# Optimization experiments

Hardware: AMD Instinct MI355X
Metric: run time of the kernel (lower is better)

The kernel has to match this reference:

```python
import jax, jax.numpy as jnp
import numpy as np

B, T, D, H = 256, 256, 384, 64  # batch, seq (BLOCK_SIZE), D_MODEL, HEAD_SIZE


def setup_inputs() -> dict:
    key = jax.random.key(0)
    k1, k2, k3, k4 = jax.random.split(key, 4)
    x = jax.random.normal(k1, (B, T, D), dtype=jnp.float32)
    # nn.Linear(D, H, bias=False): weight [H, D]; we store transposed [D, H] for x @ W
    Wq = jax.random.normal(k2, (D, H), dtype=jnp.float32) * (1.0 / np.sqrt(D))
    Wk = jax.random.normal(k3, (D, H), dtype=jnp.float32) * (1.0 / np.sqrt(D))
    Wv = jax.random.normal(k4, (D, H), dtype=jnp.float32) * (1.0 / np.sqrt(D))
    return {"x": x, "Wq": Wq, "Wk": Wk, "Wv": Wv}


def reference(x, Wq, Wk, Wv):
    # x: [B, T, D]
    q = x @ Wq  # [B, T, H]
    k = x @ Wk  # [B, T, H]
    v = x @ Wv  # [B, T, H]
    scale = 1.0 / jnp.sqrt(jnp.asarray(k.shape[-1], dtype=x.dtype))
    wei = jnp.einsum('bth,bsh->bts', q, k) * scale  # [B, T, T]
    causal = jnp.tril(jnp.ones((x.shape[1], x.shape[1]), dtype=bool))
    wei = jnp.where(causal, wei, -jnp.inf)
    wei = jax.nn.softmax(wei, axis=-1)
    # dropout is identity in eval mode (deterministic reference)
    out = jnp.einsum('bts,bsh->bth', wei, v)  # [B, T, H]
    return out
```

## Files before the change

### kernel.cpp

```cpp
#include <hip/hip_runtime.h>

#define BATCH 256
#define TT 256
#define DD 384
#define HH 64
#define SCALE 0.125f
#define SHIFT 14.0f

typedef __attribute__((ext_vector_type(8))) short short8;
typedef __attribute__((ext_vector_type(4))) float floatx4;

#define KS_STRIDE 72
#define QS_STRIDE 72
#define VT_STRIDE 264
#define PS_STRIDE 40
#define WELEMS (3 * DD * HH)

__device__ __forceinline__ unsigned short f2bf(float f) {
    unsigned int u = __float_as_uint(f);
    u += 0x7fffu + ((u >> 16) & 1u);
    return (unsigned short)(u >> 16);
}
__device__ __forceinline__ float bf2f(unsigned short u) {
    return __uint_as_float(((unsigned int)u) << 16);
}

__device__ __forceinline__ void gld_lds16(const void* g, void* ldst) {
    __builtin_amdgcn_global_load_lds(
        (__attribute__((address_space(1))) void*)(unsigned long long)g,
        (__attribute__((address_space(3))) void*)(unsigned int)(unsigned long long)ldst,
        16, 0, 0);
}

__device__ __forceinline__ short8 cvt8(float4 f0, float4 f1) {
    short8 a;
    a[0] = (short)f2bf(f0.x); a[1] = (short)f2bf(f0.y);
    a[2] = (short)f2bf(f0.z); a[3] = (short)f2bf(f0.w);
    a[4] = (short)f2bf(f1.x); a[5] = (short)f2bf(f1.y);
    a[6] = (short)f2bf(f1.z); a[7] = (short)f2bf(f1.w);
    return a;
}

__global__ void pack_w_kernel(const float* __restrict__ wq,
                              const float* __restrict__ wk,
                              const float* __restrict__ wv,
                              unsigned short* __restrict__ wf) {
    int idx = blockIdx.x * 256 + threadIdx.x;
    if (idx >= WELEMS) return;
    int j = idx & 7;
    int lane = (idx >> 3) & 63;
    int nt = (idx >> 9) & 3;
    int rem = idx >> 11;
    int mat = rem % 3;
    int ch = rem / 3;
    int l16 = lane & 15, q = lane >> 4;
    int h = 16 * nt + l16;
    int d = 32 * ch + 8 * q + j;
    const float* w = (mat == 0) ? wq : (mat == 1) ? wk : wv;
    wf[idx] = f2bf(w[d * HH + h]);
}

__global__ __launch_bounds__(512, 2)
void fused_kernel(const float* __restrict__ x, const unsigned short* __restrict__ wfrag,
                  float* __restrict__ out) {
    __shared__ __align__(16) union LdsU {
        unsigned short w[WELEMS];
        struct {
            unsigned short ks[TT * KS_STRIDE];
            unsigned short vt[HH * VT_STRIDE];
            unsigned short q[TT * QS_STRIDE];
            unsigned short p[8][16 * PS_STRIDE];
        } s;
    } U;

    const int b = blockIdx.x;
    const int tid = threadIdx.x;
    const int wave = tid >> 6;
    const int lane = tid & 63;
    const int quad = lane >> 4;
    const int l16 = lane & 15;

    const float* xb = x + (size_t)b * TT * DD;

    const float* xr0 = xb + (size_t)(32 * wave + l16) * DD + 8 * quad;
    const float* xr1 = xr0 + (size_t)16 * DD;

    floatx4 cq[2][4] = {};
    floatx4 ck[2][4] = {};
    floatx4 cv[2][4] = {};

    float4 xfA[4], xfB[4];

    xfA[0] = *(const float4*)(xr0);
    xfA[1] = *(const float4*)(xr0 + 4);
    xfA[2] = *(const float4*)(xr1);
    xfA[3] = *(const float4*)(xr1 + 4);

    #pragma unroll
    for (int t = 0; t < 18; ++t) {
        int grp = wave * 18 + t;
        gld_lds16(wfrag + (size_t)grp * 512 + lane * 8, U.w + grp * 512);
    }

    __syncthreads();

    #define GEMM_BODY(CUR, NXT, CH, PREF)                                          \
        {                                                                          \
            if (PREF) {                                                            \
                const float* p0_ = xr0 + ((CH) + 1) * 32;                          \
                const float* p1_ = xr1 + ((CH) + 1) * 32;                          \
                NXT[0] = *(const float4*)(p0_);                                    \
                NXT[1] = *(const float4*)(p0_ + 4);                                \
                NXT[2] = *(const float4*)(p1_);                                    \
                NXT[3] = *(const float4*)(p1_ + 4);                                \
            }                                                                      \
            short8 wf_[12];                                                        \
            _Pragma("unroll")                                                      \
            for (int i = 0; i < 12; ++i)                                           \
                wf_[i] = *(const short8*)(U.w + (size_t)((CH) * 12 + i) * 512 + lane * 8); \
            short8 a0 = cvt8(CUR[0], CUR[1]);                                      \
            short8 a1 = cvt8(CUR[2], CUR[3]);                                      \
            _Pragma("unroll")                                                      \
            for (int nt = 0; nt < 4; ++nt) {                                       \
                cq[0][nt] = __builtin_amdgcn_mfma_f32_16x16x32_bf16(a0, wf_[nt], cq[0][nt], 0, 0, 0);      \
                cq[1][nt] = __builtin_amdgcn_mfma_f32_16x16x32_bf16(a1, wf_[nt], cq[1][nt], 0, 0, 0);      \
                ck[0][nt] = __builtin_amdgcn_mfma_f32_16x16x32_bf16(a0, wf_[4 + nt], ck[0][nt], 0, 0, 0);  \
                ck[1][nt] = __builtin_amdgcn_mfma_f32_16x16x32_bf16(a1, wf_[4 + nt], ck[1][nt], 0, 0, 0);  \
                cv[0][nt] = __builtin_amdgcn_mfma_f32_16x16x32_bf16(a0, wf_[8 + nt], cv[0][nt], 0, 0, 0);  \
                cv[1][nt] = __builtin_amdgcn_mfma_f32_16x16x32_bf16(a1, wf_[8 + nt], cv[1][nt], 0, 0, 0);  \
            }                                                                      \
        }

    #pragma unroll 1
    for (int t = 0; t < 6; ++t) {
        GEMM_BODY(xfA, xfB, 2 * t, 1);
        GEMM_BODY(xfB, xfA, 2 * t + 1, (t < 5));
    }
    #undef GEMM_BODY

    __syncthreads();

    #pragma unroll
    for (int mi = 0; mi < 2; ++mi)
      #pragma unroll
      for (int nt = 0; nt < 4; ++nt)
        #pragma unroll
        for (int r = 0; r < 4; ++r) {
            int row = 32 * wave + 16 * mi + 4 * quad + r;
            int col = 16 * nt + l16;
            U.s.q[row * QS_STRIDE + col] = f2bf(cq[mi][nt][r]);
            U.s.ks[row * KS_STRIDE + col] = f2bf(ck[mi][nt][r]);
            U.s.vt[col * VT_STRIDE + row] = f2bf(cv[mi][nt][r]);
        }

    __syncthreads();

    floatx4 o[2][4] = {};
    float l_run[2][4] = {{0.f, 0.f, 0.f, 0.f}, {0.f, 0.f, 0.f, 0.f}};
    unsigned short* psw = U.s.p[wave];

    #pragma unroll
    for (int gi = 0; gi < 2; ++gi) {
        int g = gi ? (15 - wave) : wave;
        int gr0 = 16 * g;
        short8 aq0 = *(const short8*)(U.s.q + (size_t)(gr0 + l16) * QS_STRIDE + quad * 8);
        short8 aq1 = *(const short8*)(U.s.q + (size_t)(gr0 + l16) * QS_STRIDE + 32 + quad * 8);
        int clast = g >> 1;
        for (int c = 0; c <= clast; ++c) {
            floatx4 s[2] = {};
            #pragma unroll
            for (int ni = 0; ni < 2; ++ni) {
                const unsigned short* kbase =
                    U.s.ks + (size_t)(32 * c + 16 * ni + l16) * KS_STRIDE + quad * 8;
                s[ni] = __builtin_amdgcn_mfma_f32_16x16x32_bf16(aq0, *(const short8*)(kbase), s[ni], 0, 0, 0);
                s[ni] = __builtin_amdgcn_mfma_f32_16x16x32_bf16(aq1, *(const short8*)(kbase + 32), s[ni], 0, 0, 0);
            }
            bool partial = (c == clast);
            #pragma unroll
            for (int r = 0; r < 4; ++r) {
                int row = gr0 + 4 * quad + r;
                float p0 = __expf(s[0][r] * SCALE - SHIFT);
                float p1 = __expf(s[1][r] * SCALE - SHIFT);
                if (partial) {
                    if (32 * c + l16 > row) p0 = 0.f;
                    if (32 * c + 16 + l16 > row) p1 = 0.f;
                }
                unsigned short b0 = f2bf(p0), b1 = f2bf(p1);
                l_run[gi][r] += bf2f(b0) + bf2f(b1);
                psw[(4 * quad + r) * PS_STRIDE + l16] = b0;
                psw[(4 * quad + r) * PS_STRIDE + 16 + l16] = b1;
            }
            short8 ap = *(const short8*)(psw + l16 * PS_STRIDE + quad * 8);
            #pragma unroll
            for (int nt = 0; nt < 4; ++nt) {
                short8 bv = *(const short8*)(U.s.vt + (size_t)(16 * nt + l16) * VT_STRIDE + 32 * c + quad * 8);
                o[gi][nt] = __builtin_amdgcn_mfma_f32_16x16x32_bf16(ap, bv, o[gi][nt], 0, 0, 0);
            }
        }
    }

    float* outb = out + (size_t)b * TT * HH;
    #pragma unroll
    for (int gi = 0; gi < 2; ++gi) {
        int g = gi ? (15 - wave) : wave;
        #pragma unroll
        for (int r = 0; r < 4; ++r) {
            float l = l_run[gi][r];
            l += __shfl_xor(l, 1);
            l += __shfl_xor(l, 2);
            l += __shfl_xor(l, 4);
            l += __shfl_xor(l, 8);
            l_run[gi][r] = l;
        }
        #pragma unroll
        for (int nt = 0; nt < 4; ++nt)
          #pragma unroll
          for (int r = 0; r < 4; ++r) {
            int row = 16 * g + 4 * quad + r;
            outb[(size_t)row * HH + 16 * nt + l16] = o[gi][nt][r] / l_run[gi][r];
          }
    }
}

extern "C" void kernel_launch(void* const* d_in, const int* in_sizes, int n_in,
                              void* d_out, int out_size, void* d_ws, size_t ws_size,
                              hipStream_t stream) {
    const float* x  = (const float*)d_in[0];
    const float* wq = (const float*)d_in[1];
    const float* wk = (const float*)d_in[2];
    const float* wv = (const float*)d_in[3];
    unsigned short* wf = (unsigned short*)d_ws;
    float* o = (float*)d_out;

    pack_w_kernel<<<(WELEMS + 255) / 256, 256, 0, stream>>>(wq, wk, wv, wf);
    fused_kernel<<<BATCH, 512, 0, stream>>>(x, wf, o);
}
```

Baseline: 169.1 us.

## Fuse weight packing into main kernel and deepen x prefetch

Removes the separate weight-packing kernel launch. Each block now reads fp32 Wq/Wk/Wv straight from global memory, converts them to bf16 and writes them into the MFMA fragment layout in LDS. The x prefetch is reworked to keep two chunks in flight. The final normalization uses a reciprocal multiply instead of a divide. The cost is that all 256 blocks redo the weight conversion with strided scalar global loads, where before they did a single async global-to-LDS copy of pre-packed data.

```diff
diff --git a/kernel.cpp b/kernel.cpp
--- a/kernel.cpp
+++ b/kernel.cpp
@@ -23,13 +23,6 @@
 }
 __device__ __forceinline__ float bf2f(unsigned short u) {
     return __uint_as_float(((unsigned int)u) << 16);
-}
-
-__device__ __forceinline__ void gld_lds16(const void* g, void* ldst) {
-    __builtin_amdgcn_global_load_lds(
-        (__attribute__((address_space(1))) void*)(unsigned long long)g,
-        (__attribute__((address_space(3))) void*)(unsigned int)(unsigned long long)ldst,
-        16, 0, 0);
 }
 
 __device__ __forceinline__ short8 cvt8(float4 f0, float4 f1) {
@@ -41,27 +34,11 @@
     return a;
 }
 
-__global__ void pack_w_kernel(const float* __restrict__ wq,
-                              const float* __restrict__ wk,
-                              const float* __restrict__ wv,
-                              unsigned short* __restrict__ wf) {
-    int idx = blockIdx.x * 256 + threadIdx.x;
-    if (idx >= WELEMS) return;
-    int j = idx & 7;
-    int lane = (idx >> 3) & 63;
-    int nt = (idx >> 9) & 3;
-    int rem = idx >> 11;
-    int mat = rem % 3;
-    int ch = rem / 3;
-    int l16 = lane & 15, q = lane >> 4;
-    int h = 16 * nt + l16;
-    int d = 32 * ch + 8 * q + j;
-    const float* w = (mat == 0) ? wq : (mat == 1) ? wk : wv;
-    wf[idx] = f2bf(w[d * HH + h]);
-}
-
 __global__ __launch_bounds__(512, 2)
-void fused_kernel(const float* __restrict__ x, const unsigned short* __restrict__ wfrag,
+void fused_kernel(const float* __restrict__ x,
+                  const float* __restrict__ wq,
+                  const float* __restrict__ wk,
+                  const float* __restrict__ wv,
                   float* __restrict__ out) {
     __shared__ __align__(16) union LdsU {
         unsigned short w[WELEMS];
@@ -95,31 +72,46 @@
     xfA[1] = *(const float4*)(xr0 + 4);
     xfA[2] = *(const float4*)(xr1);
     xfA[3] = *(const float4*)(xr1 + 4);
-
-    #pragma unroll
-    for (int t = 0; t < 18; ++t) {
-        int grp = wave * 18 + t;
-        gld_lds16(wfrag + (size_t)grp * 512 + lane * 8, U.w + grp * 512);
+    xfB[0] = *(const float4*)(xr0 + 32);
+    xfB[1] = *(const float4*)(xr0 + 36);
+    xfB[2] = *(const float4*)(xr1 + 32);
+    xfB[3] = *(const float4*)(xr1 + 36);
+
+    for (int g = 0; g < 18; ++g) {
+        int gidx = g * 512 + tid;
+        int laneg = gidx & 63;
+        int nt = (gidx >> 6) & 3;
+        int rem = gidx >> 8;
+        int mat = rem % 3;
+        int ch = rem / 3;
+        int l16g = laneg & 15, qg = laneg >> 4;
+        const float* w = (mat == 0) ? wq : (mat == 1) ? wk : wv;
+        const float* src = w + (size_t)(32 * ch + 8 * qg) * HH + 16 * nt + l16g;
+        short8 pk;
+        #pragma unroll
+        for (int j = 0; j < 8; ++j)
+            pk[j] = (short)f2bf(src[(size_t)j * HH]);
+        *(short8*)(U.w + (size_t)gidx * 8) = pk;
     }
 
     __syncthreads();
 
-    #define GEMM_BODY(CUR, NXT, CH, PREF)                                          \
+    #define GEMM_BODY(BUF, CH)                                                     \
         {                                                                          \
-            if (PREF) {                                                            \
-                const float* p0_ = xr0 + ((CH) + 1) * 32;                          \
-                const float* p1_ = xr1 + ((CH) + 1) * 32;                          \
-                NXT[0] = *(const float4*)(p0_);                                    \
-                NXT[1] = *(const float4*)(p0_ + 4);                                \
-                NXT[2] = *(const float4*)(p1_);                                    \
-                NXT[3] = *(const float4*)(p1_ + 4);                                \
+            short8 a0 = cvt8(BUF[0], BUF[1]);                                      \
+            short8 a1 = cvt8(BUF[2], BUF[3]);                                      \
+            if ((CH) + 2 < 12) {                                                   \
+                const float* p0_ = xr0 + ((CH) + 2) * 32;                          \
+                const float* p1_ = xr1 + ((CH) + 2) * 32;                          \
+                BUF[0] = *(const float4*)(p0_);                                    \
+                BUF[1] = *(const float4*)(p0_ + 4);                                \
+                BUF[2] = *(const float4*)(p1_);                                    \
+                BUF[3] = *(const float4*)(p1_ + 4);                                \
             }                                                                      \
             short8 wf_[12];                                                        \
             _Pragma("unroll")                                                      \
             for (int i = 0; i < 12; ++i)                                           \
                 wf_[i] = *(const short8*)(U.w + (size_t)((CH) * 12 + i) * 512 + lane * 8); \
-            short8 a0 = cvt8(CUR[0], CUR[1]);                                      \
-            short8 a1 = cvt8(CUR[2], CUR[3]);                                      \
             _Pragma("unroll")                                                      \
             for (int nt = 0; nt < 4; ++nt) {                                       \
                 cq[0][nt] = __builtin_amdgcn_mfma_f32_16x16x32_bf16(a0, wf_[nt], cq[0][nt], 0, 0, 0);      \
@@ -133,8 +125,8 @@
 
     #pragma unroll 1
     for (int t = 0; t < 6; ++t) {
-        GEMM_BODY(xfA, xfB, 2 * t, 1);
-        GEMM_BODY(xfB, xfA, 2 * t + 1, (t < 5));
+        GEMM_BODY(xfA, 2 * t);
+        GEMM_BODY(xfB, 2 * t + 1);
     }
     #undef GEMM_BODY
 
@@ -203,6 +195,7 @@
     #pragma unroll
     for (int gi = 0; gi < 2; ++gi) {
         int g = gi ? (15 - wave) : wave;
+        float linv[4];
         #pragma unroll
         for (int r = 0; r < 4; ++r) {
             float l = l_run[gi][r];
@@ -210,14 +203,14 @@
             l += __shfl_xor(l, 2);
             l += __shfl_xor(l, 4);
             l += __shfl_xor(l, 8);
-            l_run[gi][r] = l;
+            linv[r] = 1.0f / l;
         }
         #pragma unroll
         for (int nt = 0; nt < 4; ++nt)
           #pragma unroll
           for (int r = 0; r < 4; ++r) {
             int row = 16 * g + 4 * quad + r;
-            outb[(size_t)row * HH + 16 * nt + l16] = o[gi][nt][r] / l_run[gi][r];
+            outb[(size_t)row * HH + 16 * nt + l16] = o[gi][nt][r] * linv[r];
           }
     }
 }
@@ -229,9 +222,8 @@
     const float* wq = (const float*)d_in[1];
     const float* wk = (const float*)d_in[2];
     const float* wv = (const float*)d_in[3];
-    unsigned short* wf = (unsigned short*)d_ws;
     float* o = (float*)d_out;
-
-    pack_w_kernel<<<(WELEMS + 255) / 256, 256, 0, stream>>>(wq, wk, wv, wf);
-    fused_kernel<<<BATCH, 512, 0, stream>>>(x, wf, o);
-}
+    (void)d_ws; (void)ws_size;
+
+    fused_kernel<<<BATCH, 512, 0, stream>>>(x, wq, wk, wv, o);
+}
```

Measured after the change: 176.2 us. +4.2%, slower.

## Split fused attention into separate QKV projection and attention kernels

Applied to the files above, without the earlier changes.

Replaces the single per-batch fused kernel (512 threads, whole weight matrix in LDS) with two kernels of 1024 blocks each. The QKV kernel streams weight chunks through a double-buffered LDS pipeline and writes bf16 Q, K and transposed V to workspace. The attention kernel reads them straight from global or L2 and handles one 16-row group per wave. This raises the block count and occupancy and removes the large LDS footprint, at the cost of an extra launch and a global round-trip for Q, K and V.

```diff
diff --git a/kernel.cpp b/kernel.cpp
--- a/kernel.cpp
+++ b/kernel.cpp
@@ -10,11 +10,14 @@
 typedef __attribute__((ext_vector_type(8))) short short8;
 typedef __attribute__((ext_vector_type(4))) float floatx4;
 
-#define KS_STRIDE 72
-#define QS_STRIDE 72
-#define VT_STRIDE 264
+#define WELEMS (3 * DD * HH)
+#define WCHUNK (12 * 512)
 #define PS_STRIDE 40
-#define WELEMS (3 * DD * HH)
+
+#define WF_OFF 0
+#define Q_OFF  147456
+#define K_OFF  (Q_OFF + BATCH * TT * HH * 2)
+#define VT_OFF (K_OFF + BATCH * TT * HH * 2)
 
 __device__ __forceinline__ unsigned short f2bf(float f) {
     unsigned int u = __float_as_uint(f);
@@ -60,166 +63,159 @@
     wf[idx] = f2bf(w[d * HH + h]);
 }
 
-__global__ __launch_bounds__(512, 2)
-void fused_kernel(const float* __restrict__ x, const unsigned short* __restrict__ wfrag,
-                  float* __restrict__ out) {
-    __shared__ __align__(16) union LdsU {
-        unsigned short w[WELEMS];
-        struct {
-            unsigned short ks[TT * KS_STRIDE];
-            unsigned short vt[HH * VT_STRIDE];
-            unsigned short q[TT * QS_STRIDE];
-            unsigned short p[8][16 * PS_STRIDE];
-        } s;
-    } U;
-
-    const int b = blockIdx.x;
+__global__ __launch_bounds__(256)
+void qkv_kernel(const float* __restrict__ x, const unsigned short* __restrict__ wf,
+                unsigned short* __restrict__ wsq, unsigned short* __restrict__ wsk,
+                unsigned short* __restrict__ wsv) {
+    __shared__ __align__(16) unsigned short Wbuf[2][WCHUNK];
+
+    const int B = blockIdx.x;
+    const int b = B & 255, qb = B >> 8;
     const int tid = threadIdx.x;
     const int wave = tid >> 6;
     const int lane = tid & 63;
     const int quad = lane >> 4;
     const int l16 = lane & 15;
-
-    const float* xb = x + (size_t)b * TT * DD;
-
-    const float* xr0 = xb + (size_t)(32 * wave + l16) * DD + 8 * quad;
-    const float* xr1 = xr0 + (size_t)16 * DD;
-
-    floatx4 cq[2][4] = {};
-    floatx4 ck[2][4] = {};
-    floatx4 cv[2][4] = {};
-
-    float4 xfA[4], xfB[4];
-
-    xfA[0] = *(const float4*)(xr0);
-    xfA[1] = *(const float4*)(xr0 + 4);
-    xfA[2] = *(const float4*)(xr1);
-    xfA[3] = *(const float4*)(xr1 + 4);
-
-    #pragma unroll
-    for (int t = 0; t < 18; ++t) {
-        int grp = wave * 18 + t;
-        gld_lds16(wfrag + (size_t)grp * 512 + lane * 8, U.w + grp * 512);
-    }
-
-    __syncthreads();
-
-    #define GEMM_BODY(CUR, NXT, CH, PREF)                                          \
-        {                                                                          \
-            if (PREF) {                                                            \
-                const float* p0_ = xr0 + ((CH) + 1) * 32;                          \
-                const float* p1_ = xr1 + ((CH) + 1) * 32;                          \
-                NXT[0] = *(const float4*)(p0_);                                    \
-                NXT[1] = *(const float4*)(p0_ + 4);                                \
-                NXT[2] = *(const float4*)(p1_);                                    \
-                NXT[3] = *(const float4*)(p1_ + 4);                                \
-            }                                                                      \
-            short8 wf_[12];                                                        \
-            _Pragma("unroll")                                                      \
-            for (int i = 0; i < 12; ++i)                                           \
-                wf_[i] = *(const short8*)(U.w + (size_t)((CH) * 12 + i) * 512 + lane * 8); \
-            short8 a0 = cvt8(CUR[0], CUR[1]);                                      \
-            short8 a1 = cvt8(CUR[2], CUR[3]);                                      \
-            _Pragma("unroll")                                                      \
-            for (int nt = 0; nt < 4; ++nt) {                                       \
-                cq[0][nt] = __builtin_amdgcn_mfma_f32_16x16x32_bf16(a0, wf_[nt], cq[0][nt], 0, 0, 0);      \
-                cq[1][nt] = __builtin_amdgcn_mfma_f32_16x16x32_bf16(a1, wf_[nt], cq[1][nt], 0, 0, 0);      \
-                ck[0][nt] = __builtin_amdgcn_mfma_f32_16x16x32_bf16(a0, wf_[4 + nt], ck[0][nt], 0, 0, 0);  \
-                ck[1][nt] = __builtin_amdgcn_mfma_f32_16x16x32_bf16(a1, wf_[4 + nt], ck[1][nt], 0, 0, 0);  \
-                cv[0][nt] = __builtin_amdgcn_mfma_f32_16x16x32_bf16(a0, wf_[8 + nt], cv[0][nt], 0, 0, 0);  \
-                cv[1][nt] = __builtin_amdgcn_mfma_f32_16x16x32_bf16(a1, wf_[8 + nt], cv[1][nt], 0, 0, 0);  \
-            }                                                                      \
+    const int base = 64 * qb + 16 * wave;
+
+    const float* xr = x + ((size_t)b * TT + base + l16) * DD + 8 * quad;
+
+    floatx4 cq[4] = {}, ck[4] = {}, cv[4] = {};
+    float4 xA0, xA1, xB0, xB1;
+    xA0 = *(const float4*)(xr);       xA1 = *(const float4*)(xr + 4);
+    xB0 = *(const float4*)(xr + 32);  xB1 = *(const float4*)(xr + 36);
+
+    #pragma unroll
+    for (int i = 0; i < 3; ++i)
+        gld_lds16(wf + (size_t)(256 * i + wave * 64 + lane) * 8,
+                  &Wbuf[0][(256 * i + wave * 64) * 8]);
+
+    #define QKV_BODY(X0, X1, CH)                                                    \
+        {                                                                           \
+            __syncthreads();          \
+            if ((CH) + 1 < 12) {                                                    \
+                _Pragma("unroll")                                                   \
+                for (int i = 0; i < 3; ++i)                                         \
+                    gld_lds16(wf + (size_t)((CH) + 1) * WCHUNK                      \
+                                 + (size_t)(256 * i + wave * 64 + lane) * 8,        \
+                              &Wbuf[((CH) + 1) & 1][(256 * i + wave * 64) * 8]);    \
+            }                                                                       \
+            short8 a0 = cvt8(X0, X1);                                               \
+            if ((CH) + 2 < 12) {                                                    \
+                X0 = *(const float4*)(xr + ((CH) + 2) * 32);                        \
+                X1 = *(const float4*)(xr + ((CH) + 2) * 32 + 4);                    \
+            }                                                                       \
+            const unsigned short* wb = Wbuf[(CH) & 1];                              \
+            _Pragma("unroll")                                                       \
+            for (int nt = 0; nt < 4; ++nt) {                                        \
+                short8 w0 = *(const short8*)(wb + (nt) * 512 + lane * 8);           \
+                short8 w1 = *(const short8*)(wb + (4 + nt) * 512 + lane * 8);       \
+                short8 w2 = *(const short8*)(wb + (8 + nt) * 512 + lane * 8);       \
+                cq[nt] = __builtin_amdgcn_mfma_f32_16x16x32_bf16(a0, w0, cq[nt], 0, 0, 0); \
+                ck[nt] = __builtin_amdgcn_mfma_f32_16x16x32_bf16(a0, w1, ck[nt], 0, 0, 0); \
+                cv[nt] = __builtin_amdgcn_mfma_f32_16x16x32_bf16(a0, w2, cv[nt], 0, 0, 0); \
+            }                                                                       \
         }
 
     #pragma unroll 1
     for (int t = 0; t < 6; ++t) {
-        GEMM_BODY(xfA, xfB, 2 * t, 1);
-        GEMM_BODY(xfB, xfA, 2 * t + 1, (t < 5));
+        QKV_BODY(xA0, xA1, 2 * t);
+        QKV_BODY(xB0, xB1, 2 * t + 1);
     }
-    #undef GEMM_BODY
-
-    __syncthreads();
-
-    #pragma unroll
-    for (int mi = 0; mi < 2; ++mi)
+    #undef QKV_BODY
+
+    unsigned short* qw = wsq + ((size_t)b * TT + base) * HH;
+    unsigned short* kw = wsk + ((size_t)b * TT + base) * HH;
+    unsigned short* vw = wsv + (size_t)b * HH * TT;
+    #pragma unroll
+    for (int nt = 0; nt < 4; ++nt)
       #pragma unroll
-      for (int nt = 0; nt < 4; ++nt)
+      for (int r = 0; r < 4; ++r) {
+        int rr = 4 * quad + r;
+        qw[(size_t)rr * HH + 16 * nt + l16] = f2bf(cq[nt][r]);
+        kw[(size_t)rr * HH + 16 * nt + l16] = f2bf(ck[nt][r]);
+        vw[(size_t)(16 * nt + l16) * TT + base + rr] = f2bf(cv[nt][r]);
+      }
+}
+
+__global__ __launch_bounds__(256)
+void attn_kernel(const unsigned short* __restrict__ wsq,
+                 const unsigned short* __restrict__ wsk,
+                 const unsigned short* __restrict__ wsv,
+                 float* __restrict__ out) {
+    __shared__ __align__(16) unsigned short P[4][16 * PS_STRIDE];
+
+    const int B = blockIdx.x;
+    const int b = B & 255, j = B >> 8;
+    const int tid = threadIdx.x;
+    const int wave = tid >> 6;
+    const int lane = tid & 63;
+    const int quad = lane >> 4;
+    const int l16 = lane & 15;
+    const int g = j + 4 * wave;
+    const int gr0 = 16 * g;
+
+    const unsigned short* Qb = wsq + (size_t)b * TT * HH;
+    const unsigned short* Kb = wsk + (size_t)b * TT * HH;
+    const unsigned short* Vb = wsv + (size_t)b * HH * TT;
+
+    short8 aq0 = *(const short8*)(Qb + (size_t)(gr0 + l16) * HH + 8 * quad);
+    short8 aq1 = *(const short8*)(Qb + (size_t)(gr0 + l16) * HH + 32 + 8 * quad);
+
+    floatx4 o[4] = {};
+    float l_run[4] = {0.f, 0.f, 0.f, 0.f};
+    unsigned short* psw = P[wave];
+    const int clast = g >> 1;
+
+    for (int c = 0; c <= clast; ++c) {
+        floatx4 s[2] = {};
+        #pragma unroll
+        for (int ni = 0; ni < 2; ++ni) {
+            const unsigned short* kp = Kb + (size_t)(32 * c + 16 * ni + l16) * HH + 8 * quad;
+            s[ni] = __builtin_amdgcn_mfma_f32_16x16x32_bf16(aq0, *(const short8*)(kp), s[ni], 0, 0, 0);
+            s[ni] = __builtin_amdgcn_mfma_f32_16x16x32_bf16(aq1, *(const short8*)(kp + 32), s[ni], 0, 0, 0);
+        }
+        bool partial = (c == clast);
         #pragma unroll
         for (int r = 0; r < 4; ++r) {
-            int row = 32 * wave + 16 * mi + 4 * quad + r;
-            int col = 16 * nt + l16;
-            U.s.q[row * QS_STRIDE + col] = f2bf(cq[mi][nt][r]);
-            U.s.ks[row * KS_STRIDE + col] = f2bf(ck[mi][nt][r]);
-            U.s.vt[col * VT_STRIDE + row] = f2bf(cv[mi][nt][r]);
-        }
-
-    __syncthreads();
-
-    floatx4 o[2][4] = {};
-    float l_run[2][4] = {{0.f, 0.f, 0.f, 0.f}, {0.f, 0.f, 0.f, 0.f}};
-    unsigned short* psw = U.s.p[wave];
-
-    #pragma unroll
-    for (int gi = 0; gi < 2; ++gi) {
-        int g = gi ? (15 - wave) : wave;
-        int gr0 = 16 * g;
-        short8 aq0 = *(const short8*)(U.s.q + (size_t)(gr0 + l16) * QS_STRIDE + quad * 8);
-        short8 aq1 = *(const short8*)(U.s.q + (size_t)(gr0 + l16) * QS_STRIDE + 32 + quad * 8);
-        int clast = g >> 1;
-        for (int c = 0; c <= clast; ++c) {
-            floatx4 s[2] = {};
-            #pragma unroll
-            for (int ni = 0; ni < 2; ++ni) {
-                const unsigned short* kbase =
-                    U.s.ks + (size_t)(32 * c + 16 * ni + l16) * KS_STRIDE + quad * 8;
-                s[ni] = __builtin_amdgcn_mfma_f32_16x16x32_bf16(aq0, *(const short8*)(kbase), s[ni], 0, 0, 0);
-                s[ni] = __builtin_amdgcn_mfma_f32_16x16x32_bf16(aq1, *(const short8*)(kbase + 32), s[ni], 0, 0, 0);
+            int row = gr0 + 4 * quad + r;
+            float p0 = __expf(s[0][r] * SCALE - SHIFT);
+            float p1 = __expf(s[1][r] * SCALE - SHIFT);
+            if (partial) {
+                if (32 * c + l16 > row) p0 = 0.f;
+                if (32 * c + 16 + l16 > row) p1 = 0.f;
             }
-            bool partial = (c == clast);
-            #pragma unroll
-            for (int r = 0; r < 4; ++r) {
-                int row = gr0 + 4 * quad + r;
-                float p0 = __expf(s[0][r] * SCALE - SHIFT);
-                float p1 = __expf(s[1][r] * SCALE - SHIFT);
-                if (partial) {
-                    if (32 * c + l16 > row) p0 = 0.f;
-                    if (32 * c + 16 + l16 > row) p1 = 0.f;
-                }
-                unsigned short b0 = f2bf(p0), b1 = f2bf(p1);
-                l_run[gi][r] += bf2f(b0) + bf2f(b1);
-                psw[(4 * quad + r) * PS_STRIDE + l16] = b0;
-                psw[(4 * quad + r) * PS_STRIDE + 16 + l16] = b1;
-            }
-            short8 ap = *(const short8*)(psw + l16 * PS_STRIDE + quad * 8);
-            #pragma unroll
-            for (int nt = 0; nt < 4; ++nt) {
-                short8 bv = *(const short8*)(U.s.vt + (size_t)(16 * nt + l16) * VT_STRIDE + 32 * c + quad * 8);
-                o[gi][nt] = __builtin_amdgcn_mfma_f32_16x16x32_bf16(ap, bv, o[gi][nt], 0, 0, 0);
-            }
+            unsigned short b0 = f2bf(p0), b1 = f2bf(p1);
+            l_run[r] += bf2f(b0) + bf2f(b1);
+            psw[(4 * quad + r) * PS_STRIDE + l16] = b0;
+            psw[(4 * quad + r) * PS_STRIDE + 16 + l16] = b1;
+        }
+        short8 ap = *(const short8*)(psw + l16 * PS_STRIDE + quad * 8);
+        #pragma unroll
+        for (int nt = 0; nt < 4; ++nt) {
+            short8 bv = *(const short8*)(Vb + (size_t)(16 * nt + l16) * TT + 32 * c + quad * 8);
+            o[nt] = __builtin_amdgcn_mfma_f32_16x16x32_bf16(ap, bv, o[nt], 0, 0, 0);
         }
     }
 
     float* outb = out + (size_t)b * TT * HH;
-    #pragma unroll
-    for (int gi = 0; gi < 2; ++gi) {
-        int g = gi ? (15 - wave) : wave;
-        #pragma unroll
-        for (int r = 0; r < 4; ++r) {
-            float l = l_run[gi][r];
-            l += __shfl_xor(l, 1);
-            l += __shfl_xor(l, 2);
-            l += __shfl_xor(l, 4);
-            l += __shfl_xor(l, 8);
-            l_run[gi][r] = l;
-        }
-        #pragma unroll
-        for (int nt = 0; nt < 4; ++nt)
-          #pragma unroll
-          for (int r = 0; r < 4; ++r) {
-            int row = 16 * g + 4 * quad + r;
-            outb[(size_t)row * HH + 16 * nt + l16] = o[gi][nt][r] / l_run[gi][r];
-          }
+    float linv[4];
+    #pragma unroll
+    for (int r = 0; r < 4; ++r) {
+        float l = l_run[r];
+        l += __shfl_xor(l, 1);
+        l += __shfl_xor(l, 2);
+        l += __shfl_xor(l, 4);
+        l += __shfl_xor(l, 8);
+        linv[r] = 1.0f / l;
     }
+    #pragma unroll
+    for (int nt = 0; nt < 4; ++nt)
+      #pragma unroll
+      for (int r = 0; r < 4; ++r) {
+        int row = gr0 + 4 * quad + r;
+        outb[(size_t)row * HH + 16 * nt + l16] = o[nt][r] * linv[r];
+      }
 }
 
 extern "C" void kernel_launch(void* const* d_in, const int* in_sizes, int n_in,
@@ -229,9 +225,14 @@
     const float* wq = (const float*)d_in[1];
     const float* wk = (const float*)d_in[2];
     const float* wv = (const float*)d_in[3];
-    unsigned short* wf = (unsigned short*)d_ws;
     float* o = (float*)d_out;
 
+    unsigned short* wf  = (unsigned short*)((char*)d_ws + WF_OFF);
+    unsigned short* wsq = (unsigned short*)((char*)d_ws + Q_OFF);
+    unsigned short* wsk = (unsigned short*)((char*)d_ws + K_OFF);
+    unsigned short* wsv = (unsigned short*)((char*)d_ws + VT_OFF);
+
     pack_w_kernel<<<(WELEMS + 255) / 256, 256, 0, stream>>>(wq, wk, wv, wf);
-    fused_kernel<<<BATCH, 512, 0, stream>>>(x, wf, o);
-}
+    qkv_kernel<<<BATCH * 4, 256, 0, stream>>>(x, wf, wsq, wsk, wsv);
+    attn_kernel<<<BATCH * 4, 256, 0, stream>>>(wsq, wsk, wsv, o);
+}
```

After: 189.3 us. 1.12x slower.

## Double waves per block to 16, each owning one 16-row tile

Applied to the files above, without the earlier changes.

The fused kernel now runs 1024 threads (16 waves) per batch element instead of 512. In the projection GEMM each wave computes 16 rows instead of 32, and in attention each wave handles one query tile instead of two. Query tiles are assigned to waves in a folded pattern to balance the causal work. The intent is more wavefronts in flight to hide latency, at the cost of fewer accumulators per wave, less reuse of each LDS weight fragment, and a tighter register budget under launch_bounds(1024,4). The final normalisation also changes from a per-element divide to multiplying by a reciprocal.

```diff
diff --git a/kernel.cpp b/kernel.cpp
--- a/kernel.cpp
+++ b/kernel.cpp
@@ -60,16 +60,16 @@
     wf[idx] = f2bf(w[d * HH + h]);
 }
 
-__global__ __launch_bounds__(512, 2)
+__global__ __launch_bounds__(1024, 4)
 void fused_kernel(const float* __restrict__ x, const unsigned short* __restrict__ wfrag,
                   float* __restrict__ out) {
     __shared__ __align__(16) union LdsU {
         unsigned short w[WELEMS];
         struct {
+            unsigned short q[TT * QS_STRIDE];
             unsigned short ks[TT * KS_STRIDE];
             unsigned short vt[HH * VT_STRIDE];
-            unsigned short q[TT * QS_STRIDE];
-            unsigned short p[8][16 * PS_STRIDE];
+            unsigned short p[16][16 * PS_STRIDE];
         } s;
     } U;
 
@@ -82,144 +82,131 @@
 
     const float* xb = x + (size_t)b * TT * DD;
 
-    const float* xr0 = xb + (size_t)(32 * wave + l16) * DD + 8 * quad;
-    const float* xr1 = xr0 + (size_t)16 * DD;
-
-    floatx4 cq[2][4] = {};
-    floatx4 ck[2][4] = {};
-    floatx4 cv[2][4] = {};
-
-    float4 xfA[4], xfB[4];
-
-    xfA[0] = *(const float4*)(xr0);
-    xfA[1] = *(const float4*)(xr0 + 4);
-    xfA[2] = *(const float4*)(xr1);
-    xfA[3] = *(const float4*)(xr1 + 4);
-
-    #pragma unroll
-    for (int t = 0; t < 18; ++t) {
-        int grp = wave * 18 + t;
+    const float* xr = xb + (size_t)(16 * wave + l16) * DD + 8 * quad;
+
+    floatx4 cq[4] = {}, ck[4] = {}, cv[4] = {};
+
+    float4 xf0A, xf1A, xf0B, xf1B;
+    xf0A = *(const float4*)(xr);       xf1A = *(const float4*)(xr + 4);
+    xf0B = *(const float4*)(xr + 32);  xf1B = *(const float4*)(xr + 36);
+
+    #pragma unroll
+    for (int t = 0; t < 9; ++t) {
+        int grp = wave * 9 + t;
         gld_lds16(wfrag + (size_t)grp * 512 + lane * 8, U.w + grp * 512);
     }
 
     __syncthreads();
 
-    #define GEMM_BODY(CUR, NXT, CH, PREF)                                          \
+    #define GEMM_BODY(X0, X1, CH)                                                  \
         {                                                                          \
-            if (PREF) {                                                            \
-                const float* p0_ = xr0 + ((CH) + 1) * 32;                          \
-                const float* p1_ = xr1 + ((CH) + 1) * 32;                          \
-                NXT[0] = *(const float4*)(p0_);                                    \
-                NXT[1] = *(const float4*)(p0_ + 4);                                \
-                NXT[2] = *(const float4*)(p1_);                                    \
-                NXT[3] = *(const float4*)(p1_ + 4);                                \
+            short8 a0 = cvt8(X0, X1);                                              \
+            if ((CH) + 2 < 12) {                                                   \
+                X0 = *(const float4*)(xr + ((CH) + 2) * 32);                       \
+                X1 = *(const float4*)(xr + ((CH) + 2) * 32 + 4);                   \
             }                                                                      \
-            short8 wf_[12];                                                        \
+            const unsigned short* wb = U.w + (size_t)(CH) * 12 * 512 + lane * 8;   \
             _Pragma("unroll")                                                      \
-            for (int i = 0; i < 12; ++i)                                           \
-                wf_[i] = *(const short8*)(U.w + (size_t)((CH) * 12 + i) * 512 + lane * 8); \
-            short8 a0 = cvt8(CUR[0], CUR[1]);                                      \
-            short8 a1 = cvt8(CUR[2], CUR[3]);                                      \
-            _Pragma("unroll")                                                      \
-            for (int nt = 0; nt < 4; ++nt) {                                       \
-                cq[0][nt] = __builtin_amdgcn_mfma_f32_16x16x32_bf16(a0, wf_[nt], cq[0][nt], 0, 0, 0);      \
-                cq[1][nt] = __builtin_amdgcn_mfma_f32_16x16x32_bf16(a1, wf_[nt], cq[1][nt], 0, 0, 0);      \
-                ck[0][nt] = __builtin_amdgcn_mfma_f32_16x16x32_bf16(a0, wf_[4 + nt], ck[0][nt], 0, 0, 0);  \
-                ck[1][nt] = __builtin_amdgcn_mfma_f32_16x16x32_bf16(a1, wf_[4 + nt], ck[1][nt], 0, 0, 0);  \
-                cv[0][nt] = __builtin_amdgcn_mfma_f32_16x16x32_bf16(a0, wf_[8 + nt], cv[0][nt], 0, 0, 0);  \
-                cv[1][nt] = __builtin_amdgcn_mfma_f32_16x16x32_bf16(a1, wf_[8 + nt], cv[1][nt], 0, 0, 0);  \
+            for (int h = 0; h < 2; ++h) {                                          \
+                short8 fq0 = *(const short8*)(wb + (0 * 4 + 2 * h + 0) * 512);     \
+                short8 fq1 = *(const short8*)(wb + (0 * 4 + 2 * h + 1) * 512);     \
+                short8 fk0 = *(const short8*)(wb + (1 * 4 + 2 * h + 0) * 512);     \
+                short8 fk1 = *(const short8*)(wb + (1 * 4 + 2 * h + 1) * 512);     \
+                short8 fv0 = *(const short8*)(wb + (2 * 4 + 2 * h + 0) * 512);     \
+                short8 fv1 = *(const short8*)(wb + (2 * 4 + 2 * h + 1) * 512);     \
+                cq[2 * h]     = __builtin_amdgcn_mfma_f32_16x16x32_bf16(a0, fq0, cq[2 * h], 0, 0, 0);     \
+                cq[2 * h + 1] = __builtin_amdgcn_mfma_f32_16x16x32_bf16(a0, fq1, cq[2 * h + 1], 0, 0, 0); \
+                ck[2 * h]     = __builtin_amdgcn_mfma_f32_16x16x32_bf16(a0, fk0, ck[2 * h], 0, 0, 0);     \
+                ck[2 * h + 1] = __builtin_amdgcn_mfma_f32_16x16x32_bf16(a0, fk1, ck[2 * h + 1], 0, 0, 0); \
+                cv[2 * h]     = __builtin_amdgcn_mfma_f32_16x16x32_bf16(a0, fv0, cv[2 * h], 0, 0, 0);     \
+                cv[2 * h + 1] = __builtin_amdgcn_mfma_f32_16x16x32_bf16(a0, fv1, cv[2 * h + 1], 0, 0, 0); \
             }                                                                      \
         }
 
     #pragma unroll 1
     for (int t = 0; t < 6; ++t) {
-        GEMM_BODY(xfA, xfB, 2 * t, 1);
-        GEMM_BODY(xfB, xfA, 2 * t + 1, (t < 5));
+        GEMM_BODY(xf0A, xf1A, 2 * t);
+        GEMM_BODY(xf0B, xf1B, 2 * t + 1);
     }
     #undef GEMM_BODY
 
     __syncthreads();
 
     #pragma unroll
-    for (int mi = 0; mi < 2; ++mi)
+    for (int nt = 0; nt < 4; ++nt)
       #pragma unroll
-      for (int nt = 0; nt < 4; ++nt)
+      for (int r = 0; r < 4; ++r) {
+          int row = 16 * wave + 4 * quad + r;
+          int col = 16 * nt + l16;
+          U.s.q[row * QS_STRIDE + col] = f2bf(cq[nt][r]);
+          U.s.ks[row * KS_STRIDE + col] = f2bf(ck[nt][r]);
+          U.s.vt[col * VT_STRIDE + row] = f2bf(cv[nt][r]);
+      }
+
+    __syncthreads();
+
+    int g = wave;
+    if (wave & 4) g = (wave & 8) ? (27 - wave) : (11 - wave);
+    const int gr0 = 16 * g;
+
+    floatx4 o[4] = {};
+    float l_run[4] = {0.f, 0.f, 0.f, 0.f};
+    unsigned short* psw = U.s.p[wave];
+
+    short8 aq0 = *(const short8*)(U.s.q + (size_t)(gr0 + l16) * QS_STRIDE + quad * 8);
+    short8 aq1 = *(const short8*)(U.s.q + (size_t)(gr0 + l16) * QS_STRIDE + 32 + quad * 8);
+    const int clast = g >> 1;
+
+    for (int c = 0; c <= clast; ++c) {
+        floatx4 s[2] = {};
+        #pragma unroll
+        for (int ni = 0; ni < 2; ++ni) {
+            const unsigned short* kbase =
+                U.s.ks + (size_t)(32 * c + 16 * ni + l16) * KS_STRIDE + quad * 8;
+            s[ni] = __builtin_amdgcn_mfma_f32_16x16x32_bf16(aq0, *(const short8*)(kbase), s[ni], 0, 0, 0);
+            s[ni] = __builtin_amdgcn_mfma_f32_16x16x32_bf16(aq1, *(const short8*)(kbase + 32), s[ni], 0, 0, 0);
+        }
+        bool partial = (c == clast);
         #pragma unroll
         for (int r = 0; r < 4; ++r) {
-            int row = 32 * wave + 16 * mi + 4 * quad + r;
-            int col = 16 * nt + l16;
-            U.s.q[row * QS_STRIDE + col] = f2bf(cq[mi][nt][r]);
-            U.s.ks[row * KS_STRIDE + col] = f2bf(ck[mi][nt][r]);
-            U.s.vt[col * VT_STRIDE + row] = f2bf(cv[mi][nt][r]);
-        }
-
-    __syncthreads();
-
-    floatx4 o[2][4] = {};
-    float l_run[2][4] = {{0.f, 0.f, 0.f, 0.f}, {0.f, 0.f, 0.f, 0.f}};
-    unsigned short* psw = U.s.p[wave];
-
-    #pragma unroll
-    for (int gi = 0; gi < 2; ++gi) {
-        int g = gi ? (15 - wave) : wave;
-        int gr0 = 16 * g;
-        short8 aq0 = *(const short8*)(U.s.q + (size_t)(gr0 + l16) * QS_STRIDE + quad * 8);
-        short8 aq1 = *(const short8*)(U.s.q + (size_t)(gr0 + l16) * QS_STRIDE + 32 + quad * 8);
-        int clast = g >> 1;
-        for (int c = 0; c <= clast; ++c) {
-            floatx4 s[2] = {};
-            #pragma unroll
-            for (int ni = 0; ni < 2; ++ni) {
-                const unsigned short* kbase =
-                    U.s.ks + (size_t)(32 * c + 16 * ni + l16) * KS_STRIDE + quad * 8;
-                s[ni] = __builtin_amdgcn_mfma_f32_16x16x32_bf16(aq0, *(const short8*)(kbase), s[ni], 0, 0, 0);
-                s[ni] = __builtin_amdgcn_mfma_f32_16x16x32_bf16(aq1, *(const short8*)(kbase + 32), s[ni], 0, 0, 0);
+            int row = gr0 + 4 * quad + r;
+            float p0 = __expf(s[0][r] * SCALE - SHIFT);
+            float p1 = __expf(s[1][r] * SCALE - SHIFT);
+            if (partial) {
+                if (32 * c + l16 > row) p0 = 0.f;
+                if (32 * c + 16 + l16 > row) p1 = 0.f;
             }
-            bool partial = (c == clast);
-            #pragma unroll
-            for (int r = 0; r < 4; ++r) {
-                int row = gr0 + 4 * quad + r;
-                float p0 = __expf(s[0][r] * SCALE - SHIFT);
-                float p1 = __expf(s[1][r] * SCALE - SHIFT);
-                if (partial) {
-                    if (32 * c + l16 > row) p0 = 0.f;
-                    if (32 * c + 16 + l16 > row) p1 = 0.f;
-                }
-                unsigned short b0 = f2bf(p0), b1 = f2bf(p1);
-                l_run[gi][r] += bf2f(b0) + bf2f(b1);
-                psw[(4 * quad + r) * PS_STRIDE + l16] = b0;
-                psw[(4 * quad + r) * PS_STRIDE + 16 + l16] = b1;
-            }
-            short8 ap = *(const short8*)(psw + l16 * PS_STRIDE + quad * 8);
-            #pragma unroll
-            for (int nt = 0; nt < 4; ++nt) {
-                short8 bv = *(const short8*)(U.s.vt + (size_t)(16 * nt + l16) * VT_STRIDE + 32 * c + quad * 8);
-                o[gi][nt] = __builtin_amdgcn_mfma_f32_16x16x32_bf16(ap, bv, o[gi][nt], 0, 0, 0);
-            }
+            unsigned short b0 = f2bf(p0), b1 = f2bf(p1);
+            l_run[r] += bf2f(b0) + bf2f(b1);
+            psw[(4 * quad + r) * PS_STRIDE + l16] = b0;
+            psw[(4 * quad + r) * PS_STRIDE + 16 + l16] = b1;
+        }
+        short8 ap = *(const short8*)(psw + l16 * PS_STRIDE + quad * 8);
+        #pragma unroll
+        for (int nt = 0; nt < 4; ++nt) {
+            short8 bv = *(const short8*)(U.s.vt + (size_t)(16 * nt + l16) * VT_STRIDE + 32 * c + quad * 8);
+            o[nt] = __builtin_amdgcn_mfma_f32_16x16x32_bf16(ap, bv, o[nt], 0, 0, 0);
         }
     }
 
     float* outb = out + (size_t)b * TT * HH;
-    #pragma unroll
-    for (int gi = 0; gi < 2; ++gi) {
-        int g = gi ? (15 - wave) : wave;
-        #pragma unroll
-        for (int r = 0; r < 4; ++r) {
-            float l = l_run[gi][r];
-            l += __shfl_xor(l, 1);
-            l += __shfl_xor(l, 2);
-            l += __shfl_xor(l, 4);
-            l += __shfl_xor(l, 8);
-            l_run[gi][r] = l;
-        }
-        #pragma unroll
-        for (int nt = 0; nt < 4; ++nt)
-          #pragma unroll
-          for (int r = 0; r < 4; ++r) {
-            int row = 16 * g + 4 * quad + r;
-            outb[(size_t)row * HH + 16 * nt + l16] = o[gi][nt][r] / l_run[gi][r];
-          }
-    }
+    float linv[4];
+    #pragma unroll
+    for (int r = 0; r < 4; ++r) {
+        float l = l_run[r];
+        l += __shfl_xor(l, 1);
+        l += __shfl_xor(l, 2);
+        l += __shfl_xor(l, 4);
+        l += __shfl_xor(l, 8);
+        linv[r] = 1.0f / l;
+    }
+    #pragma unroll
+    for (int nt = 0; nt < 4; ++nt)
+      #pragma unroll
+      for (int r = 0; r < 4; ++r) {
+        int row = gr0 + 4 * quad + r;
+        outb[(size_t)row * HH + 16 * nt + l16] = o[nt][r] * linv[r];
+      }
 }
 
 extern "C" void kernel_launch(void* const* d_in, const int* in_sizes, int n_in,
@@ -233,5 +220,5 @@
     float* o = (float*)d_out;
 
     pack_w_kernel<<<(WELEMS + 255) / 256, 256, 0, stream>>>(wq, wk, wv, wf);
-    fused_kernel<<<BATCH, 512, 0, stream>>>(x, wf, o);
-}
+    fused_kernel<<<BATCH, 1024, 0, stream>>>(x, wf, o);
+}
```

Result: no change. 170.2 us (+0.7%).
